# Optimization experiments

Hardware: AMD Instinct MI355X
Metric: run time of the kernel (lower is better)

Reference implementation:

```python
import jax, jax.numpy as jnp
import numpy as np
from functools import partial

SIZES = (32.0, 64.0, 128.0, 256.0, 512.0)
RATIOS = (0.5, 1.0, 2.0)
POS_T, NEG_T = 0.7, 0.3


def _make_anchors(img_size, grid_sizes):
    # Mirrors AnchorGenerator: per feature, per size, per ratio, grid-flattened.
    parts = []
    for g in grid_sizes:
        stride = img_size / g
        steps = jnp.arange(g, dtype=jnp.float32) * stride
        x, y = jnp.meshgrid(steps, steps, indexing='ij')  # torch default 'ij'
        for s in SIZES:
            for r in RATIOS:
                rs = float(np.sqrt(r))
                wa = jnp.full((g, g), s * rs, jnp.float32)
                ha = jnp.full((g, g), s / rs, jnp.float32)
                parts.append(jnp.stack((x, y, wa, ha), axis=-1).reshape(-1, 4))
    return jnp.concatenate(parts, axis=0)  # [R,4] (cx,cy,w,h)


def _conv(x, w, b, pad):
    y = jax.lax.conv_general_dilated(x, w, (1, 1), [(pad, pad), (pad, pad)],
                                     dimension_numbers=('NCHW', 'OIHW', 'NCHW'))
    return y + b[None, :, None, None]


def _head(feat, conv_w, conv_b, cls_w, cls_b, box_w, box_b):
    t = jax.nn.relu(_conv(feat, conv_w, conv_b, 1))
    logits = _conv(t, cls_w, cls_b, 0)   # [b,A,g,g]
    bbox = _conv(t, box_w, box_b, 0)     # [b,4A,g,g]
    b, A, g, _ = logits.shape
    logits = logits.reshape(b, -1)       # [b, A*g*g] (anchor-major, matches anchor order)
    bbox = bbox.reshape(b, A, 4, g, g).transpose(0, 1, 3, 4, 2).reshape(b, -1, 4)
    return logits, bbox


def _iou(a, b):
    # a [R,4] xyxy, b [N,4] xyxy -> [R,N]
    lt = jnp.maximum(a[:, None, :2], b[None, :, :2])
    rb = jnp.minimum(a[:, None, 2:], b[None, :, 2:])
    wh = jnp.clip(rb - lt, 0.0)
    inter = wh[..., 0] * wh[..., 1]
    area_a = (a[:, 2] - a[:, 0]) * (a[:, 3] - a[:, 1])
    area_b = (b[:, 2] - b[:, 0]) * (b[:, 3] - b[:, 1])
    return inter / (area_a[:, None] + area_b[None, :] - inter)


def _label_one(anchors_xyxy, gt_xywh):
    # label_anchors for a single image
    gt = jnp.concatenate([gt_xywh[:, :2], gt_xywh[:, :2] + gt_xywh[:, 2:]], axis=-1)
    iou = _iou(anchors_xyxy, gt)               # [R,N]
    score = iou.max(axis=1)
    matched = gt[jnp.argmax(iou, axis=1)]      # [R,4]
    pos = score > POS_T
    pos = pos.at[jnp.argmax(iou, axis=0)].set(True)  # best anchor per gt
    labels = jnp.where(score < NEG_T, 0.0, jnp.where(pos, 1.0, -1.0))
    return labels, matched


def _forward(images, feats, gt_boxes, conv_w, conv_b, cls_w, cls_b, box_w, box_b):
    grid_sizes = [f.shape[-1] for f in feats]
    anchors = _make_anchors(float(images.shape[-1]), grid_sizes)  # [R,4] cwh
    half = anchors[:, 2:] * 0.5
    anchors_xyxy = jnp.concatenate([anchors[:, :2] - half, anchors[:, :2] + half], -1)
    outs = [_head(f, conv_w, conv_b, cls_w, cls_b, box_w, box_b) for f in feats]
    obj = jnp.concatenate([o for o, _ in outs], axis=1)      # [b,R]
    deltas = jnp.concatenate([d for _, d in outs], axis=1)   # [b,R,4]
    labels, matched = jax.vmap(partial(_label_one, anchors_xyxy))(gt_boxes)
    preds = jnp.concatenate([obj[..., None], deltas], axis=-1)  # [b,R,5]
    return preds, labels, matched


def setup_inputs() -> dict:
    key = jax.random.key(0)
    ks = jax.random.split(key, 12)
    b, C, A = 2, 256, 15
    grids = (128, 64, 32, 16, 8)
    inp = {'images': jax.random.uniform(ks[0], (b, 3, 512, 512), jnp.float32)}
    for i, g in enumerate(grids):
        inp[f'feat{i}'] = jax.random.normal(ks[1 + i], (b, C, g, g), jnp.float32)
    xy = jax.random.uniform(ks[6], (b, 32, 2), jnp.float32) * 384.0
    wh = 16.0 + jax.random.uniform(ks[7], (b, 32, 2), jnp.float32) * 112.0
    inp['gt_boxes'] = jnp.concatenate([xy, wh], axis=-1)  # (x,y,w,h)
    inp['conv_w'] = 0.01 * jax.random.normal(ks[8], (C, C, 3, 3), jnp.float32)
    inp['conv_b'] = jnp.zeros((C,), jnp.float32)
    inp['cls_w'] = 0.01 * jax.random.normal(ks[9], (A, C, 1, 1), jnp.float32)
    inp['cls_b'] = jnp.zeros((A,), jnp.float32)
    inp['box_w'] = 0.01 * jax.random.normal(ks[10], (4 * A, C, 1, 1), jnp.float32)
    inp['box_b'] = jnp.zeros((4 * A,), jnp.float32)
    return inp


def reference(images, feat0, feat1, feat2, feat3, feat4, gt_boxes,
              conv_w, conv_b, cls_w, cls_b, box_w, box_b):
    return _forward(images, [feat0, feat1, feat2, feat3, feat4], gt_boxes,
                    conv_w, conv_b, cls_w, cls_b, box_w, box_b)
```

## Files before the change

kernel.cpp:

```cpp
#include <hip/hip_runtime.h>

typedef unsigned short u16;
typedef unsigned char  u8;
typedef unsigned int   u32;
typedef __bf16 bf16x8 __attribute__((ext_vector_type(8)));
typedef float  f32x4  __attribute__((ext_vector_type(4)));
typedef u16    u16x8  __attribute__((ext_vector_type(8)));
typedef u16    u16x4  __attribute__((ext_vector_type(4)));

#define R_TOTAL 327360
#define LAB_OFF 3273600
#define MAT_OFF 3928320
#define NLBLK   1279

static __device__ const int    D_LOG2G[5] = {7, 6, 5, 4, 3};
static __device__ const size_t D_FTOFF[5] = {0, 8389120, 10486784, 11011584, 11143168};
static __device__ const int    D_TPOFF[5] = {0, 32768, 40960, 43008, 43520};
static __device__ const int    D_AOFF[5]  = {0, 245760, 307200, 322560, 326400};

static __device__ const float D_WH[15][2] = {
  {22.627416997969522f, 45.254833995939045f}, {32.f, 32.f},   {45.254833995939045f, 22.627416997969522f},
  {45.254833995939045f, 90.50966799187809f},  {64.f, 64.f},   {90.50966799187809f, 45.254833995939045f},
  {90.50966799187809f, 181.01933598375618f},  {128.f, 128.f}, {181.01933598375618f, 90.50966799187809f},
  {181.01933598375618f, 362.03867196751236f}, {256.f, 256.f}, {362.03867196751236f, 181.01933598375618f},
  {362.03867196751236f, 724.0773439350247f},  {512.f, 512.f}, {724.0773439350247f, 362.03867196751236f},
};

__device__ __forceinline__ u16 f2bf(float x) {
  u32 u = __float_as_uint(x);
  u32 r = u + 0x7FFFu + ((u >> 16) & 1u);
  return (u16)(r >> 16);
}
__device__ __forceinline__ float bf2f(u16 v) { return __uint_as_float(((u32)v) << 16); }

__device__ __forceinline__ void glds16(const void* g, void* l) {
  __builtin_amdgcn_global_load_lds(
      (const __attribute__((address_space(1))) u32*)g,
      (__attribute__((address_space(3))) u32*)l, 16, 0, 0);
}

__device__ inline void anchor_box(int r, float& x1, float& y1, float& x2, float& y2) {
  #pragma clang fp contract(off)
  int off, lg;
  if (r < 245760)      { off = 0;      lg = 7; }
  else if (r < 307200) { off = 245760; lg = 6; }
  else if (r < 322560) { off = 307200; lg = 5; }
  else if (r < 326400) { off = 322560; lg = 4; }
  else                 { off = 326400; lg = 3; }
  int rem  = r - off;
  int a    = rem >> (2 * lg);
  int rem2 = rem & ((1 << (2 * lg)) - 1);
  int i = rem2 >> lg;
  int j = rem2 & ((1 << lg) - 1);
  float stride = (float)(512 >> lg);
  float cx = (float)i * stride;
  float cy = (float)j * stride;
  float hw = D_WH[a][0] * 0.5f;
  float hh = D_WH[a][1] * 0.5f;
  x1 = cx - hw; y1 = cy - hh; x2 = cx + hw; y2 = cy + hh;
}

__device__ inline float iou_f(float ax1, float ay1, float ax2, float ay2,
                              float bx1, float by1, float bx2, float by2) {
  #pragma clang fp contract(off)
  float ltx = fmaxf(ax1, bx1), lty = fmaxf(ay1, by1);
  float rbx = fminf(ax2, bx2), rby = fminf(ay2, by2);
  float iw = fmaxf(rbx - ltx, 0.f);
  float ih = fmaxf(rby - lty, 0.f);
  float inter = iw * ih;
  float aa = (ax2 - ax1) * (ay2 - ay1);
  float ab = (bx2 - bx1) * (by2 - by1);
  return inter / (aa + ab - inter);
}

__global__ __launch_bounds__(256) void pack_all_kernel(
    const float* __restrict__ cw, u16* __restrict__ wp,
    const float* __restrict__ cls_w, const float* __restrict__ cls_b,
    const float* __restrict__ box_w, const float* __restrict__ box_b,
    u16* __restrict__ Wb, float* __restrict__ hbias) {
  if (blockIdx.x < 2304) {
    int idx = blockIdx.x * 256 + threadIdx.x;
    int ks  = idx >> 13;
    int rem = idx & 8191;
    int co  = rem >> 5;
    int k   = rem & 31;
    int tap = ks >> 3;
    int cb  = ks & 7;
    float v = cw[co * 2304 + (cb * 32 + k) * 9 + tap];
    int qd = k >> 3, wi = k & 7;
    int dq = qd ^ ((co >> 1) & 3);
    wp[(size_t)ks * 8192 + co * 32 + dq * 8 + wi] = f2bf(v);
  } else {
    int idx = (blockIdx.x - 2304) * 256 + threadIdx.x;
    int row = idx >> 8, k = idx & 255;
    float v = (row < 15) ? cls_w[row * 256 + k] : (row < 75) ? box_w[(row - 15) * 256 + k] : 0.f;
    Wb[row * 256 + k] = f2bf(v);
    if (idx < 80) hbias[idx] = (idx < 15) ? cls_b[idx] : (idx < 75) ? box_b[idx - 15] : 0.f;
  }
}

__global__ __launch_bounds__(256) void feat_pack_kernel(
    const float* __restrict__ f0, const float* __restrict__ f1,
    const float* __restrict__ f2, const float* __restrict__ f3,
    const float* __restrict__ f4, u16* __restrict__ Ft) {
  __shared__ float tile[64][65];
  int bid = blockIdx.x;
  int l, base, nb1;
  if (bid < 514)      { l = 0; base = 0;   nb1 = 257; }
  else if (bid < 644) { l = 1; base = 514; nb1 = 65; }
  else if (bid < 678) { l = 2; base = 644; nb1 = 17; }
  else if (bid < 688) { l = 3; base = 678; nb1 = 5; }
  else                { l = 4; base = 688; nb1 = 2; }
  const int lg = D_LOG2G[l];
  const int HW = 1 << (2 * lg);
  int blk = bid - base;
  int b   = blk / nb1;
  int p0  = (blk - b * nb1) * 64;
  u16* dst = Ft + D_FTOFF[l];
  const int tid = threadIdx.x;
  if (p0 >= HW) {
    if (tid < 32) {
      u16x8 z = (u16x8)0;
      *(u16x8*)(dst + ((size_t)b * (HW + 1) + HW) * 256 + tid * 8) = z;
    }
    return;
  }
  const float* fsel = (l == 0) ? f0 : (l == 1) ? f1 : (l == 2) ? f2 : (l == 3) ? f3 : f4;
  const float* fb = fsel + (size_t)b * 256 * HW;
  for (int cg = 0; cg < 4; ++cg) {
    __syncthreads();
    #pragma unroll
    for (int i = 0; i < 16; ++i) {
      int idx = i * 256 + tid;
      int cl = idx >> 6, pp = idx & 63;
      tile[cl][pp] = fb[(size_t)(cg * 64 + cl) * HW + p0 + pp];
    }
    __syncthreads();
    #pragma unroll
    for (int i = 0; i < 2; ++i) {
      int slot = i * 256 + tid;
      int pos = slot >> 3, ch = slot & 7;
      u16x8 v;
      #pragma unroll
      for (int j = 0; j < 8; ++j) v[j] = f2bf(tile[ch * 8 + j][pos]);
      *(u16x8*)(dst + ((size_t)b * (HW + 1) + p0 + pos) * 256 + cg * 64 + ch * 8) = v;
    }
  }
}

__global__ __launch_bounds__(128) void conv_mfma_kernel(
    const u16* __restrict__ Ft, const u16* __restrict__ wp,
    const float* __restrict__ cb, u16* __restrict__ tP) {
  __shared__ __align__(16) u8 Asb[16384];
  __shared__ __align__(16) u8 Bsb[8192];
  const int bid = blockIdx.x;
  int l, base;
  if (bid < 1024)      { l = 0; base = 0; }
  else if (bid < 1280) { l = 1; base = 1024; }
  else if (bid < 1344) { l = 2; base = 1280; }
  else if (bid < 1360) { l = 3; base = 1344; }
  else                 { l = 4; base = 1360; }
  const int lg = D_LOG2G[l];
  const int g = 1 << lg, HW = 1 << (2 * lg);
  const int lognt = 2 * lg - 5;
  const int blk = bid - base;
  const int ct = blk >> lognt;
  const int tile = blk & ((1 << lognt) - 1);
  const int n0 = tile << 6;
  const int co0 = ct << 7;
  const int tid = threadIdx.x;
  const int wv = tid >> 6, lane = tid & 63;
  const u16* FtL = Ft + D_FTOFF[l];
  const u8* wpb = (const u8*)wp;
  const int b_img = n0 >> (2 * lg);
  const int dq = tid & 3;
  const int nl0 = tid >> 2, nl1 = nl0 + 32;
  const int swz0 = (dq ^ ((nl0 >> 1) & 3)) << 3;
  const int swz1 = (dq ^ ((nl1 >> 1) & 3)) << 3;
  const int pg0 = (n0 + nl0) & (HW - 1);
  const int h0 = pg0 >> lg, w0 = pg0 & (g - 1);
  const int pg1 = (n0 + nl1) & (HW - 1);
  const int h1 = pg1 >> lg, w1 = pg1 & (g - 1);
  const u16* bimg = FtL + (size_t)b_img * (HW + 1) * 256;
  const int lm = lane & 15, lq = lane >> 4;
  int aoffs[4], boffs[4];
  #pragma unroll
  for (int mi = 0; mi < 4; ++mi) {
    int row = wv * 64 + mi * 16 + lm;
    aoffs[mi] = row * 64 + ((lq ^ ((row >> 1) & 3)) << 4);
  }
  #pragma unroll
  for (int ni = 0; ni < 4; ++ni) {
    int col = ni * 16 + lm;
    boffs[ni] = col * 64 + ((lq ^ ((col >> 1) & 3)) << 4);
  }
  f32x4 acc[4][4];
  #pragma unroll
  for (int mi = 0; mi < 4; ++mi)
    #pragma unroll
    for (int ni = 0; ni < 4; ++ni) acc[mi][ni] = (f32x4)0.f;

  auto tap_src = [&](int tap, const u16*& s0, const u16*& s1) {
    const int dh = tap / 3 - 1, dw = tap % 3 - 1;
    int sh0 = h0 + dh, sw0 = w0 + dw;
    int r0 = ((unsigned)sh0 < (unsigned)g && (unsigned)sw0 < (unsigned)g) ? (sh0 * g + sw0) : HW;
    int sh1 = h1 + dh, sw1 = w1 + dw;
    int r1 = ((unsigned)sh1 < (unsigned)g && (unsigned)sw1 < (unsigned)g) ? (sh1 * g + sw1) : HW;
    s0 = bimg + (size_t)r0 * 256 + swz0;
    s1 = bimg + (size_t)r1 * 256 + swz1;
  };
  auto STAGE = [&](int p, int tap_, int cb8_, const u16* s0, const u16* s1) {
    glds16(s0 + cb8_ * 32, Bsb + p * 4096 + wv * 1024);
    glds16(s1 + cb8_ * 32, Bsb + p * 4096 + (2 + wv) * 1024);
    const u8* aK = wpb + (size_t)(tap_ * 8 + cb8_) * 16384 + co0 * 64;
    #pragma unroll
    for (int c = 0; c < 4; ++c) {
      int ch = c * 2 + wv;
      glds16(aK + ch * 1024 + lane * 16, Asb + p * 8192 + ch * 1024);
    }
  };

  const u16 *cs0, *cs1;
  tap_src(0, cs0, cs1);
  int p = 0;
  STAGE(0, 0, 0, cs0, cs1);
  __syncthreads();

  for (int tap = 0; tap < 9; ++tap) {
    const u16 *ns0 = cs0, *ns1 = cs1;
    if (tap < 8) tap_src(tap + 1, ns0, ns1);
    #pragma unroll
    for (int cb8 = 0; cb8 < 8; ++cb8) {
      if (!(tap == 8 && cb8 == 7)) {
        if (cb8 < 7) STAGE(p ^ 1, tap, cb8 + 1, cs0, cs1);
        else         STAGE(p ^ 1, tap + 1, 0, ns0, ns1);
      }
      bf16x8 af[4], bfr[4];
      #pragma unroll
      for (int mi = 0; mi < 4; ++mi) af[mi] = *(const bf16x8*)(Asb + p * 8192 + aoffs[mi]);
      #pragma unroll
      for (int ni = 0; ni < 4; ++ni) bfr[ni] = *(const bf16x8*)(Bsb + p * 4096 + boffs[ni]);
      #pragma unroll
      for (int mi = 0; mi < 4; ++mi)
        #pragma unroll
        for (int ni = 0; ni < 4; ++ni)
          acc[mi][ni] = __builtin_amdgcn_mfma_f32_16x16x32_bf16(af[mi], bfr[ni], acc[mi][ni], 0, 0, 0);
      __syncthreads();
      p ^= 1;
    }
    cs0 = ns0; cs1 = ns1;
  }
  u16* tPL = tP + ((size_t)D_TPOFF[l] + (size_t)b_img * HW) * 256;
  #pragma unroll
  for (int mi = 0; mi < 4; ++mi) {
    const int cob = co0 + wv * 64 + mi * 16 + lq * 4;
    const float4 bs = *(const float4*)&cb[cob];
    #pragma unroll
    for (int ni = 0; ni < 4; ++ni) {
      int pp = (n0 + ni * 16 + lm) & (HW - 1);
      u16x4 v;
      v[0] = f2bf(fmaxf(acc[mi][ni][0] + bs.x, 0.f));
      v[1] = f2bf(fmaxf(acc[mi][ni][1] + bs.y, 0.f));
      v[2] = f2bf(fmaxf(acc[mi][ni][2] + bs.z, 0.f));
      v[3] = f2bf(fmaxf(acc[mi][ni][3] + bs.w, 0.f));
      *(u16x4*)&tPL[(size_t)pp * 256 + cob] = v;
    }
  }
}

__global__ __launch_bounds__(128) void head_mfma_kernel(
    const u16* __restrict__ tP, const u16* __restrict__ Wb,
    const float* __restrict__ hbias, float* __restrict__ out) {
  __shared__ __align__(16) u8 Bsb[32768];
  const int bid = blockIdx.x;
  int l, base;
  if (bid < 512)      { l = 0; base = 0; }
  else if (bid < 640) { l = 1; base = 512; }
  else if (bid < 672) { l = 2; base = 640; }
  else if (bid < 680) { l = 3; base = 672; }
  else                { l = 4; base = 680; }
  const int lg = D_LOG2G[l];
  const int HW = 1 << (2 * lg);
  const int blk = bid - base;
  const int n0 = blk << 6;
  const int tid = threadIdx.x;
  const int wv = tid >> 6, lane = tid & 63;
  const int lm = lane & 15, lq = lane >> 4;
  const u16* src = tP + ((size_t)D_TPOFF[l] + n0) * 256;
  #pragma unroll
  for (int i = 0; i < 16; ++i) {
    int c = wv + i * 2;
    int slot = c * 64 + lane;
    int pos = slot >> 5, sp = slot & 31;
    glds16(src + (size_t)pos * 256 + ((sp ^ (pos & 7)) << 3), Bsb + c * 1024);
  }
  __syncthreads();
  f32x4 acc[5][2];
  #pragma unroll
  for (int mi = 0; mi < 5; ++mi) { acc[mi][0] = (f32x4)0.f; acc[mi][1] = (f32x4)0.f; }
  for (int kb = 0; kb < 8; ++kb) {
    bf16x8 af[5], bfr[2];
    #pragma unroll
    for (int mi = 0; mi < 5; ++mi)
      af[mi] = *(const bf16x8*)&Wb[(mi * 16 + lm) * 256 + kb * 32 + lq * 8];
    #pragma unroll
    for (int ni = 0; ni < 2; ++ni) {
      int p_ = wv * 32 + ni * 16 + lm;
      bfr[ni] = *(const bf16x8*)(Bsb + p_ * 512 + (((kb * 4 + lq) ^ (p_ & 7)) << 4));
    }
    #pragma unroll
    for (int mi = 0; mi < 5; ++mi)
      #pragma unroll
      for (int ni = 0; ni < 2; ++ni)
        acc[mi][ni] = __builtin_amdgcn_mfma_f32_16x16x32_bf16(af[mi], bfr[ni], acc[mi][ni], 0, 0, 0);
  }
  const int b   = n0 >> (2 * lg);
  const int pgb = n0 & (HW - 1);
  const size_t obase = (size_t)b * R_TOTAL;
  const int aoff = D_AOFF[l];
  #pragma unroll
  for (int mi = 0; mi < 5; ++mi) {
    #pragma unroll
    for (int r = 0; r < 4; ++r) {
      int oc = mi * 16 + lq * 4 + r;
      if (oc < 75) {
        float bs = hbias[oc];
        size_t rr; int comp;
        if (oc < 15) { rr = (size_t)aoff + (size_t)oc * HW; comp = 0; }
        else { int o2 = oc - 15; rr = (size_t)aoff + (size_t)(o2 >> 2) * HW; comp = 1 + (o2 & 3); }
        #pragma unroll
        for (int ni = 0; ni < 2; ++ni) {
          int pg = pgb + wv * 32 + ni * 16 + lm;
          out[(obase + rr + pg) * 5 + comp] = acc[mi][ni][r] + bs;
        }
      }
    }
  }
}

__global__ __launch_bounds__(256) void label_fused_kernel(const float* __restrict__ gt,
                                                          float* __restrict__ out,
                                                          float2* __restrict__ partial) {
  #pragma clang fp contract(off)
  __shared__ float gx[32][4];
  __shared__ float sh[256][33];
  __shared__ float2 red[32][8];
  const int b = blockIdx.y;
  const int tid = threadIdx.x;
  if (tid < 32) {
    const float* gp = gt + ((size_t)b * 32 + tid) * 4;
    float x = gp[0], y = gp[1], w = gp[2], h = gp[3];
    gx[tid][0] = x; gx[tid][1] = y; gx[tid][2] = x + w; gx[tid][3] = y + h;
  }
  __syncthreads();
  const int r = blockIdx.x * 256 + tid;
  const bool valid = (r < R_TOTAL);
  const int rv = valid ? r : 0;
  float ax1, ay1, ax2, ay2;
  anchor_box(rv, ax1, ay1, ax2, ay2);
  float best = -1e30f; int bi = 0;
  for (int n = 0; n < 32; ++n) {
    float v = iou_f(ax1, ay1, ax2, ay2, gx[n][0], gx[n][1], gx[n][2], gx[n][3]);
    sh[tid][n] = valid ? v : -1e30f;
    if (v > best) { best = v; bi = n; }
  }
  if (valid) {
    float lab = (best < 0.3f) ? 0.f : ((best > 0.7f) ? 1.f : -1.f);
    out[LAB_OFF + (size_t)b * R_TOTAL + r] = lab;
    float4 m; m.x = gx[bi][0]; m.y = gx[bi][1]; m.z = gx[bi][2]; m.w = gx[bi][3];
    *(float4*)&out[MAT_OFF + ((size_t)b * R_TOTAL + r) * 4] = m;
  }
  __syncthreads();
  const int n = tid & 31, gr = tid >> 5;
  float bv = -1e30f; int li = 0;
  #pragma unroll 4
  for (int a = 0; a < 32; ++a) {
    int la = gr * 32 + a;
    float v = sh[la][n];
    if (v > bv) { bv = v; li = la; }
  }
  red[n][gr] = make_float2(bv, __int_as_float(li));
  __syncthreads();
  if (tid < 32) {
    float fv = -1e30f; int fi = 0;
    #pragma unroll
    for (int g2 = 0; g2 < 8; ++g2) {
      float2 pv = red[tid][g2];
      int ii = __float_as_int(pv.y);
      if (pv.x > fv) { fv = pv.x; fi = ii; }
    }
    partial[(size_t)(b * 32 + tid) * NLBLK + blockIdx.x] =
        make_float2(fv, __int_as_float(blockIdx.x * 256 + fi));
  }
}

__global__ __launch_bounds__(256) void argmax_final2_kernel(
    const float* __restrict__ gt, const float2* __restrict__ partial,
    float* __restrict__ out) {
  #pragma clang fp contract(off)
  __shared__ float sv[256];
  __shared__ int   si[256];
  const int b = blockIdx.x >> 5, n = blockIdx.x & 31;
  const float2* pp = partial + (size_t)(b * 32 + n) * NLBLK;
  const int tid = threadIdx.x;
  float bv = -1e30f; int bi = 0x7fffffff;
  for (int i = tid; i < NLBLK; i += 256) {
    float2 pv = pp[i]; int ii = __float_as_int(pv.y);
    if (pv.x > bv || (pv.x == bv && ii < bi)) { bv = pv.x; bi = ii; }
  }
  sv[tid] = bv; si[tid] = bi;
  __syncthreads();
  for (int s = 128; s > 0; s >>= 1) {
    if (tid < s) {
      float v2 = sv[tid + s]; int i2 = si[tid + s];
      if (v2 > sv[tid] || (v2 == sv[tid] && i2 < si[tid])) { sv[tid] = v2; si[tid] = i2; }
    }
    __syncthreads();
  }
  if (tid == 0) {
    int banch = si[0];
    float ax1, ay1, ax2, ay2;
    anchor_box(banch, ax1, ay1, ax2, ay2);
    float score = -1e30f;
    for (int n2 = 0; n2 < 32; ++n2) {
      const float* gp = gt + ((size_t)b * 32 + n2) * 4;
      float v = iou_f(ax1, ay1, ax2, ay2, gp[0], gp[1], gp[0] + gp[2], gp[1] + gp[3]);
      score = fmaxf(score, v);
    }
    out[LAB_OFF + (size_t)b * R_TOTAL + banch] = (score < 0.3f) ? 0.f : 1.f;
  }
}

extern "C" void kernel_launch(void* const* d_in, const int* in_sizes, int n_in,
                              void* d_out, int out_size, void* d_ws, size_t ws_size,
                              hipStream_t stream) {
  const float* f0     = (const float*)d_in[1];
  const float* f1     = (const float*)d_in[2];
  const float* f2     = (const float*)d_in[3];
  const float* f3     = (const float*)d_in[4];
  const float* f4     = (const float*)d_in[5];
  const float* gt     = (const float*)d_in[6];
  const float* conv_w = (const float*)d_in[7];
  const float* conv_b = (const float*)d_in[8];
  const float* cls_w  = (const float*)d_in[9];
  const float* cls_b  = (const float*)d_in[10];
  const float* box_w  = (const float*)d_in[11];
  const float* box_b  = (const float*)d_in[12];
  float* out = (float*)d_out;
  u8* wsb = (u8*)d_ws;

  u16*    wp      = (u16*)wsb;
  u16*    Ft      = (u16*)(wsb + 1179648);
  u16*    tP      = (u16*)(wsb + 23532544);
  u16*    Wb      = (u16*)(wsb + 45880320);
  float*  hbias   = (float*)(wsb + 45921280);
  float2* partial = (float2*)(wsb + 45921600);

  pack_all_kernel<<<2384, 256, 0, stream>>>(conv_w, wp, cls_w, cls_b, box_w, box_b, Wb, hbias);
  feat_pack_kernel<<<692, 256, 0, stream>>>(f0, f1, f2, f3, f4, Ft);
  conv_mfma_kernel<<<1364, 128, 0, stream>>>(Ft, wp, conv_b, tP);
  head_mfma_kernel<<<682, 128, 0, stream>>>(tP, Wb, hbias, out);
  label_fused_kernel<<<dim3(NLBLK, 2), 256, 0, stream>>>(gt, out, partial);
  argmax_final2_kernel<<<64, 256, 0, stream>>>(gt, partial, out);
}
```

Baseline: 231.6 us.

## Enlarge conv tile to 128x128 with 4 waves and merge prep kernels

The conv MFMA kernel moves from 128 threads computing a 128x64 output tile to 256 threads (2x2 waves) computing a 128x128 tile. The B pixel tile can now span both images, so each pixel row tracks its own image index. This halves the block count and reuses each staged weight tile across twice as many pixels, cutting global weight traffic per output. The weight-pack and feature-pack kernels are also merged into one launch to save a launch gap. The cost is fewer blocks (682) to fill the GPU's compute units and larger LDS use per block.

```diff
diff --git a/kernel.cpp b/kernel.cpp
--- a/kernel.cpp
+++ b/kernel.cpp
@@ -73,13 +73,18 @@
   return inter / (aa + ab - inter);
 }
 
-__global__ __launch_bounds__(256) void pack_all_kernel(
+__global__ __launch_bounds__(256) void prep_kernel(
     const float* __restrict__ cw, u16* __restrict__ wp,
     const float* __restrict__ cls_w, const float* __restrict__ cls_b,
     const float* __restrict__ box_w, const float* __restrict__ box_b,
-    u16* __restrict__ Wb, float* __restrict__ hbias) {
+    u16* __restrict__ Wb, float* __restrict__ hbias,
+    const float* __restrict__ f0, const float* __restrict__ f1,
+    const float* __restrict__ f2, const float* __restrict__ f3,
+    const float* __restrict__ f4, u16* __restrict__ Ft) {
+  __shared__ float tile[64][65];
+  const int tid = threadIdx.x;
   if (blockIdx.x < 2304) {
-    int idx = blockIdx.x * 256 + threadIdx.x;
+    int idx = blockIdx.x * 256 + tid;
     int ks  = idx >> 13;
     int rem = idx & 8191;
     int co  = rem >> 5;
@@ -90,21 +95,17 @@
     int qd = k >> 3, wi = k & 7;
     int dq = qd ^ ((co >> 1) & 3);
     wp[(size_t)ks * 8192 + co * 32 + dq * 8 + wi] = f2bf(v);
-  } else {
-    int idx = (blockIdx.x - 2304) * 256 + threadIdx.x;
+    return;
+  }
+  if (blockIdx.x < 2384) {
+    int idx = (blockIdx.x - 2304) * 256 + tid;
     int row = idx >> 8, k = idx & 255;
     float v = (row < 15) ? cls_w[row * 256 + k] : (row < 75) ? box_w[(row - 15) * 256 + k] : 0.f;
     Wb[row * 256 + k] = f2bf(v);
     if (idx < 80) hbias[idx] = (idx < 15) ? cls_b[idx] : (idx < 75) ? box_b[idx - 15] : 0.f;
-  }
-}
-
-__global__ __launch_bounds__(256) void feat_pack_kernel(
-    const float* __restrict__ f0, const float* __restrict__ f1,
-    const float* __restrict__ f2, const float* __restrict__ f3,
-    const float* __restrict__ f4, u16* __restrict__ Ft) {
-  __shared__ float tile[64][65];
-  int bid = blockIdx.x;
+    return;
+  }
+  int bid = blockIdx.x - 2384;
   int l, base, nb1;
   if (bid < 514)      { l = 0; base = 0;   nb1 = 257; }
   else if (bid < 644) { l = 1; base = 514; nb1 = 65; }
@@ -117,7 +118,6 @@
   int b   = blk / nb1;
   int p0  = (blk - b * nb1) * 64;
   u16* dst = Ft + D_FTOFF[l];
-  const int tid = threadIdx.x;
   if (p0 >= HW) {
     if (tid < 32) {
       u16x8 z = (u16x8)0;
@@ -148,50 +148,53 @@
   }
 }
 
-__global__ __launch_bounds__(128) void conv_mfma_kernel(
+__global__ __launch_bounds__(256) void conv_mfma_kernel(
     const u16* __restrict__ Ft, const u16* __restrict__ wp,
     const float* __restrict__ cb, u16* __restrict__ tP) {
   __shared__ __align__(16) u8 Asb[16384];
-  __shared__ __align__(16) u8 Bsb[8192];
+  __shared__ __align__(16) u8 Bsb[16384];
   const int bid = blockIdx.x;
   int l, base;
-  if (bid < 1024)      { l = 0; base = 0; }
-  else if (bid < 1280) { l = 1; base = 1024; }
-  else if (bid < 1344) { l = 2; base = 1280; }
-  else if (bid < 1360) { l = 3; base = 1344; }
-  else                 { l = 4; base = 1360; }
+  if (bid < 512)      { l = 0; base = 0; }
+  else if (bid < 640) { l = 1; base = 512; }
+  else if (bid < 672) { l = 2; base = 640; }
+  else if (bid < 680) { l = 3; base = 672; }
+  else                { l = 4; base = 680; }
   const int lg = D_LOG2G[l];
   const int g = 1 << lg, HW = 1 << (2 * lg);
-  const int lognt = 2 * lg - 5;
+  const int lognt = 2 * lg - 6;
   const int blk = bid - base;
   const int ct = blk >> lognt;
   const int tile = blk & ((1 << lognt) - 1);
-  const int n0 = tile << 6;
+  const int n0 = tile << 7;
   const int co0 = ct << 7;
   const int tid = threadIdx.x;
   const int wv = tid >> 6, lane = tid & 63;
+  const int wr = wv >> 1, wc = wv & 1;
   const u16* FtL = Ft + D_FTOFF[l];
   const u8* wpb = (const u8*)wp;
-  const int b_img = n0 >> (2 * lg);
-  const int dq = tid & 3;
-  const int nl0 = tid >> 2, nl1 = nl0 + 32;
-  const int swz0 = (dq ^ ((nl0 >> 1) & 3)) << 3;
-  const int swz1 = (dq ^ ((nl1 >> 1) & 3)) << 3;
-  const int pg0 = (n0 + nl0) & (HW - 1);
-  const int h0 = pg0 >> lg, w0 = pg0 & (g - 1);
-  const int pg1 = (n0 + nl1) & (HW - 1);
-  const int h1 = pg1 >> lg, w1 = pg1 & (g - 1);
-  const u16* bimg = FtL + (size_t)b_img * (HW + 1) * 256;
+  const int dq = lane & 3;
+  const int rB0 = wv * 32 + (lane >> 2);
+  const int rB1 = rB0 + 16;
+  int bI0, h0, w0, bI1, h1, w1, q0, q1;
+  {
+    int pf0 = n0 + rB0; bI0 = pf0 >> (2 * lg); int p0_ = pf0 & (HW - 1);
+    h0 = p0_ >> lg; w0 = p0_ & (g - 1); q0 = dq ^ ((rB0 >> 1) & 3);
+    int pf1 = n0 + rB1; bI1 = pf1 >> (2 * lg); int p1_ = pf1 & (HW - 1);
+    h1 = p1_ >> lg; w1 = p1_ & (g - 1); q1 = dq ^ ((rB1 >> 1) & 3);
+  }
+  const size_t img0 = (size_t)bI0 * (HW + 1), img1 = (size_t)bI1 * (HW + 1);
+  const u8* pA = wpb + (size_t)co0 * 64 + (size_t)(wv * 32 + (lane >> 2)) * 64 + dq * 16;
   const int lm = lane & 15, lq = lane >> 4;
   int aoffs[4], boffs[4];
   #pragma unroll
   for (int mi = 0; mi < 4; ++mi) {
-    int row = wv * 64 + mi * 16 + lm;
+    int row = wr * 64 + mi * 16 + lm;
     aoffs[mi] = row * 64 + ((lq ^ ((row >> 1) & 3)) << 4);
   }
   #pragma unroll
   for (int ni = 0; ni < 4; ++ni) {
-    int col = ni * 16 + lm;
+    int col = wc * 64 + ni * 16 + lm;
     boffs[ni] = col * 64 + ((lq ^ ((col >> 1) & 3)) << 4);
   }
   f32x4 acc[4][4];
@@ -206,18 +209,15 @@
     int r0 = ((unsigned)sh0 < (unsigned)g && (unsigned)sw0 < (unsigned)g) ? (sh0 * g + sw0) : HW;
     int sh1 = h1 + dh, sw1 = w1 + dw;
     int r1 = ((unsigned)sh1 < (unsigned)g && (unsigned)sw1 < (unsigned)g) ? (sh1 * g + sw1) : HW;
-    s0 = bimg + (size_t)r0 * 256 + swz0;
-    s1 = bimg + (size_t)r1 * 256 + swz1;
+    s0 = FtL + (img0 + r0) * 256 + q0 * 8;
+    s1 = FtL + (img1 + r1) * 256 + q1 * 8;
   };
-  auto STAGE = [&](int p, int tap_, int cb8_, const u16* s0, const u16* s1) {
-    glds16(s0 + cb8_ * 32, Bsb + p * 4096 + wv * 1024);
-    glds16(s1 + cb8_ * 32, Bsb + p * 4096 + (2 + wv) * 1024);
-    const u8* aK = wpb + (size_t)(tap_ * 8 + cb8_) * 16384 + co0 * 64;
-    #pragma unroll
-    for (int c = 0; c < 4; ++c) {
-      int ch = c * 2 + wv;
-      glds16(aK + ch * 1024 + lane * 16, Asb + p * 8192 + ch * 1024);
-    }
+  auto STAGE = [&](int p, int ks, int cb8, const u16* s0, const u16* s1) {
+    glds16(s0 + cb8 * 32, Bsb + p * 8192 + wv * 2048);
+    glds16(s1 + cb8 * 32, Bsb + p * 8192 + wv * 2048 + 1024);
+    const u8* aK = pA + (size_t)ks * 16384;
+    glds16(aK,        Asb + p * 8192 + wv * 2048);
+    glds16(aK + 1024, Asb + p * 8192 + wv * 2048 + 1024);
   };
 
   const u16 *cs0, *cs1;
@@ -232,14 +232,14 @@
     #pragma unroll
     for (int cb8 = 0; cb8 < 8; ++cb8) {
       if (!(tap == 8 && cb8 == 7)) {
-        if (cb8 < 7) STAGE(p ^ 1, tap, cb8 + 1, cs0, cs1);
-        else         STAGE(p ^ 1, tap + 1, 0, ns0, ns1);
+        if (cb8 < 7) STAGE(p ^ 1, tap * 8 + cb8 + 1, cb8 + 1, cs0, cs1);
+        else         STAGE(p ^ 1, (tap + 1) * 8, 0, ns0, ns1);
       }
       bf16x8 af[4], bfr[4];
       #pragma unroll
       for (int mi = 0; mi < 4; ++mi) af[mi] = *(const bf16x8*)(Asb + p * 8192 + aoffs[mi]);
       #pragma unroll
-      for (int ni = 0; ni < 4; ++ni) bfr[ni] = *(const bf16x8*)(Bsb + p * 4096 + boffs[ni]);
+      for (int ni = 0; ni < 4; ++ni) bfr[ni] = *(const bf16x8*)(Bsb + p * 8192 + boffs[ni]);
       #pragma unroll
       for (int mi = 0; mi < 4; ++mi)
         #pragma unroll
@@ -250,20 +250,22 @@
     }
     cs0 = ns0; cs1 = ns1;
   }
-  u16* tPL = tP + ((size_t)D_TPOFF[l] + (size_t)b_img * HW) * 256;
+  const u16* tPL = tP + (size_t)D_TPOFF[l] * 256;
   #pragma unroll
   for (int mi = 0; mi < 4; ++mi) {
-    const int cob = co0 + wv * 64 + mi * 16 + lq * 4;
+    const int cob = co0 + wr * 64 + mi * 16 + lq * 4;
     const float4 bs = *(const float4*)&cb[cob];
     #pragma unroll
     for (int ni = 0; ni < 4; ++ni) {
-      int pp = (n0 + ni * 16 + lm) & (HW - 1);
+      int pf = n0 + wc * 64 + ni * 16 + lm;
+      int bI = pf >> (2 * lg);
+      int pp = pf & (HW - 1);
       u16x4 v;
       v[0] = f2bf(fmaxf(acc[mi][ni][0] + bs.x, 0.f));
       v[1] = f2bf(fmaxf(acc[mi][ni][1] + bs.y, 0.f));
       v[2] = f2bf(fmaxf(acc[mi][ni][2] + bs.z, 0.f));
       v[3] = f2bf(fmaxf(acc[mi][ni][3] + bs.w, 0.f));
-      *(u16x4*)&tPL[(size_t)pp * 256 + cob] = v;
+      *(u16x4*)&((u16*)tPL)[((size_t)bI * HW + pp) * 256 + cob] = v;
     }
   }
 }
@@ -456,9 +458,9 @@
   float*  hbias   = (float*)(wsb + 45921280);
   float2* partial = (float2*)(wsb + 45921600);
 
-  pack_all_kernel<<<2384, 256, 0, stream>>>(conv_w, wp, cls_w, cls_b, box_w, box_b, Wb, hbias);
-  feat_pack_kernel<<<692, 256, 0, stream>>>(f0, f1, f2, f3, f4, Ft);
-  conv_mfma_kernel<<<1364, 128, 0, stream>>>(Ft, wp, conv_b, tP);
+  prep_kernel<<<3076, 256, 0, stream>>>(conv_w, wp, cls_w, cls_b, box_w, box_b,
+                                        Wb, hbias, f0, f1, f2, f3, f4, Ft);
+  conv_mfma_kernel<<<682, 256, 0, stream>>>(Ft, wp, conv_b, tP);
   head_mfma_kernel<<<682, 128, 0, stream>>>(tP, Wb, hbias, out);
   label_fused_kernel<<<dim3(NLBLK, 2), 256, 0, stream>>>(gt, out, partial);
   argmax_final2_kernel<<<64, 256, 0, stream>>>(gt, partial, out);
```

New measurement: 270.3 us. +16.7%, slower.

## Merge prep, feature pack and labeling into one launch; widen conv blocks

Applied to the files above, without the earlier changes.

The weight packing, feature transpose/pack and anchor labeling kernels become one launch partitioned by block index. The separate argmax-final kernel is replaced by 64-bit atomicMax keys plus a last-block-done counter, which needs a small memset per call. The conv kernel moves from 128 to 256 threads with a 2x2 wave layout, so each wave computes a 64x32 sub-tile and stages fewer global-to-LDS loads. The aim is to cut launch count and tail idle time and to improve conv occupancy, at the cost of atomic contention and a changed argmax tie-break (smallest index wins via complemented key).

```diff
diff --git a/kernel.cpp b/kernel.cpp
--- a/kernel.cpp
+++ b/kernel.cpp
@@ -3,6 +3,7 @@
 typedef unsigned short u16;
 typedef unsigned char  u8;
 typedef unsigned int   u32;
+typedef unsigned long long u64;
 typedef __bf16 bf16x8 __attribute__((ext_vector_type(8)));
 typedef float  f32x4  __attribute__((ext_vector_type(4)));
 typedef u16    u16x8  __attribute__((ext_vector_type(8)));
@@ -31,7 +32,6 @@
   u32 r = u + 0x7FFFu + ((u >> 16) & 1u);
   return (u16)(r >> 16);
 }
-__device__ __forceinline__ float bf2f(u16 v) { return __uint_as_float(((u32)v) << 16); }
 
 __device__ __forceinline__ void glds16(const void* g, void* l) {
   __builtin_amdgcn_global_load_lds(
@@ -73,13 +73,28 @@
   return inter / (aa + ab - inter);
 }
 
-__global__ __launch_bounds__(256) void pack_all_kernel(
+__global__ __launch_bounds__(256) void prep_label_kernel(
     const float* __restrict__ cw, u16* __restrict__ wp,
     const float* __restrict__ cls_w, const float* __restrict__ cls_b,
     const float* __restrict__ box_w, const float* __restrict__ box_b,
-    u16* __restrict__ Wb, float* __restrict__ hbias) {
+    u16* __restrict__ Wb, float* __restrict__ hbias,
+    const float* __restrict__ f0, const float* __restrict__ f1,
+    const float* __restrict__ f2, const float* __restrict__ f3,
+    const float* __restrict__ f4, u16* __restrict__ Ft,
+    const float* __restrict__ gt, float* __restrict__ out,
+    u64* __restrict__ win, u32* __restrict__ done) {
+  __shared__ union {
+    float tile[64][65];
+    struct {
+      float gx[32][4];
+      float sh[256][33];
+      float2 red[32][8];
+    } L;
+  } sm;
+  __shared__ int lastFlag;
+  const int tid = threadIdx.x;
   if (blockIdx.x < 2304) {
-    int idx = blockIdx.x * 256 + threadIdx.x;
+    int idx = blockIdx.x * 256 + tid;
     int ks  = idx >> 13;
     int rem = idx & 8191;
     int co  = rem >> 5;
@@ -90,65 +105,138 @@
     int qd = k >> 3, wi = k & 7;
     int dq = qd ^ ((co >> 1) & 3);
     wp[(size_t)ks * 8192 + co * 32 + dq * 8 + wi] = f2bf(v);
-  } else {
-    int idx = (blockIdx.x - 2304) * 256 + threadIdx.x;
+    return;
+  }
+  if (blockIdx.x < 2384) {
+    int idx = (blockIdx.x - 2304) * 256 + tid;
     int row = idx >> 8, k = idx & 255;
     float v = (row < 15) ? cls_w[row * 256 + k] : (row < 75) ? box_w[(row - 15) * 256 + k] : 0.f;
     Wb[row * 256 + k] = f2bf(v);
     if (idx < 80) hbias[idx] = (idx < 15) ? cls_b[idx] : (idx < 75) ? box_b[idx - 15] : 0.f;
-  }
-}
-
-__global__ __launch_bounds__(256) void feat_pack_kernel(
-    const float* __restrict__ f0, const float* __restrict__ f1,
-    const float* __restrict__ f2, const float* __restrict__ f3,
-    const float* __restrict__ f4, u16* __restrict__ Ft) {
-  __shared__ float tile[64][65];
-  int bid = blockIdx.x;
-  int l, base, nb1;
-  if (bid < 514)      { l = 0; base = 0;   nb1 = 257; }
-  else if (bid < 644) { l = 1; base = 514; nb1 = 65; }
-  else if (bid < 678) { l = 2; base = 644; nb1 = 17; }
-  else if (bid < 688) { l = 3; base = 678; nb1 = 5; }
-  else                { l = 4; base = 688; nb1 = 2; }
-  const int lg = D_LOG2G[l];
-  const int HW = 1 << (2 * lg);
-  int blk = bid - base;
-  int b   = blk / nb1;
-  int p0  = (blk - b * nb1) * 64;
-  u16* dst = Ft + D_FTOFF[l];
-  const int tid = threadIdx.x;
-  if (p0 >= HW) {
+    return;
+  }
+  if (blockIdx.x < 3076) {
+    int bid = blockIdx.x - 2384;
+    int l, base, nb1;
+    if (bid < 514)      { l = 0; base = 0;   nb1 = 257; }
+    else if (bid < 644) { l = 1; base = 514; nb1 = 65; }
+    else if (bid < 678) { l = 2; base = 644; nb1 = 17; }
+    else if (bid < 688) { l = 3; base = 678; nb1 = 5; }
+    else                { l = 4; base = 688; nb1 = 2; }
+    const int lg = D_LOG2G[l];
+    const int HW = 1 << (2 * lg);
+    int blk = bid - base;
+    int b   = blk / nb1;
+    int p0  = (blk - b * nb1) * 64;
+    u16* dst = Ft + D_FTOFF[l];
+    if (p0 >= HW) {
+      if (tid < 32) {
+        u16x8 z = (u16x8)0;
+        *(u16x8*)(dst + ((size_t)b * (HW + 1) + HW) * 256 + tid * 8) = z;
+      }
+      return;
+    }
+    const float* fsel = (l == 0) ? f0 : (l == 1) ? f1 : (l == 2) ? f2 : (l == 3) ? f3 : f4;
+    const float* fb = fsel + (size_t)b * 256 * HW;
+    for (int cg = 0; cg < 4; ++cg) {
+      __syncthreads();
+      #pragma unroll
+      for (int i = 0; i < 16; ++i) {
+        int idx = i * 256 + tid;
+        int cl = idx >> 6, pp = idx & 63;
+        sm.tile[cl][pp] = fb[(size_t)(cg * 64 + cl) * HW + p0 + pp];
+      }
+      __syncthreads();
+      #pragma unroll
+      for (int i = 0; i < 2; ++i) {
+        int slot = i * 256 + tid;
+        int pos = slot >> 3, ch = slot & 7;
+        u16x8 v;
+        #pragma unroll
+        for (int j = 0; j < 8; ++j) v[j] = f2bf(sm.tile[ch * 8 + j][pos]);
+        *(u16x8*)(dst + ((size_t)b * (HW + 1) + p0 + pos) * 256 + cg * 64 + ch * 8) = v;
+      }
+    }
+    return;
+  }
+  {
+    #pragma clang fp contract(off)
+    const int lb = blockIdx.x - 3076;
+    const int b = (lb >= NLBLK) ? 1 : 0;
+    const int lblk = lb - b * NLBLK;
     if (tid < 32) {
-      u16x8 z = (u16x8)0;
-      *(u16x8*)(dst + ((size_t)b * (HW + 1) + HW) * 256 + tid * 8) = z;
-    }
-    return;
-  }
-  const float* fsel = (l == 0) ? f0 : (l == 1) ? f1 : (l == 2) ? f2 : (l == 3) ? f3 : f4;
-  const float* fb = fsel + (size_t)b * 256 * HW;
-  for (int cg = 0; cg < 4; ++cg) {
+      const float* gp = gt + ((size_t)b * 32 + tid) * 4;
+      float x = gp[0], y = gp[1], w = gp[2], h = gp[3];
+      sm.L.gx[tid][0] = x; sm.L.gx[tid][1] = y;
+      sm.L.gx[tid][2] = x + w; sm.L.gx[tid][3] = y + h;
+    }
     __syncthreads();
-    #pragma unroll
-    for (int i = 0; i < 16; ++i) {
-      int idx = i * 256 + tid;
-      int cl = idx >> 6, pp = idx & 63;
-      tile[cl][pp] = fb[(size_t)(cg * 64 + cl) * HW + p0 + pp];
+    const int r = lblk * 256 + tid;
+    const bool valid = (r < R_TOTAL);
+    const int rv = valid ? r : 0;
+    float ax1, ay1, ax2, ay2;
+    anchor_box(rv, ax1, ay1, ax2, ay2);
+    float best = -1e30f; int bi = 0;
+    for (int n = 0; n < 32; ++n) {
+      float v = iou_f(ax1, ay1, ax2, ay2, sm.L.gx[n][0], sm.L.gx[n][1], sm.L.gx[n][2], sm.L.gx[n][3]);
+      sm.L.sh[tid][n] = valid ? v : -1e30f;
+      if (v > best) { best = v; bi = n; }
+    }
+    if (valid) {
+      float lab = (best < 0.3f) ? 0.f : ((best > 0.7f) ? 1.f : -1.f);
+      out[LAB_OFF + (size_t)b * R_TOTAL + r] = lab;
+      float4 m; m.x = sm.L.gx[bi][0]; m.y = sm.L.gx[bi][1];
+      m.z = sm.L.gx[bi][2]; m.w = sm.L.gx[bi][3];
+      *(float4*)&out[MAT_OFF + ((size_t)b * R_TOTAL + r) * 4] = m;
     }
     __syncthreads();
-    #pragma unroll
-    for (int i = 0; i < 2; ++i) {
-      int slot = i * 256 + tid;
-      int pos = slot >> 3, ch = slot & 7;
-      u16x8 v;
-      #pragma unroll
-      for (int j = 0; j < 8; ++j) v[j] = f2bf(tile[ch * 8 + j][pos]);
-      *(u16x8*)(dst + ((size_t)b * (HW + 1) + p0 + pos) * 256 + cg * 64 + ch * 8) = v;
-    }
-  }
-}
-
-__global__ __launch_bounds__(128) void conv_mfma_kernel(
+    const int n = tid & 31, gr = tid >> 5;
+    float bv = -1e30f; int li = 0;
+    #pragma unroll 4
+    for (int a = 0; a < 32; ++a) {
+      int la = gr * 32 + a;
+      float v = sm.L.sh[la][n];
+      if (v > bv) { bv = v; li = la; }
+    }
+    sm.L.red[n][gr] = make_float2(bv, __int_as_float(li));
+    __syncthreads();
+    if (tid < 32) {
+      float fv = -1e30f; int fi = 0;
+      #pragma unroll
+      for (int g2 = 0; g2 < 8; ++g2) {
+        float2 pv = sm.L.red[tid][g2];
+        int ii = __float_as_int(pv.y);
+        if (pv.x > fv) { fv = pv.x; fi = ii; }
+      }
+      u64 key = ((u64)__float_as_uint(fv) << 32) |
+                (u64)(0xFFFFFFFFu - (u32)(lblk * 256 + fi));
+      atomicMax(&win[b * 32 + tid], key);
+    }
+    __threadfence();
+    __syncthreads();
+    if (tid == 0) {
+      u32 old = atomicAdd(&done[b], 1u);
+      lastFlag = (old == NLBLK - 1) ? 1 : 0;
+    }
+    __syncthreads();
+    if (lastFlag && tid < 32) {
+      u64 k = atomicMax(&win[b * 32 + tid], 0ull);
+      u32 hi = (u32)(k >> 32);
+      int ra = hi ? (int)(0xFFFFFFFFu - (u32)k) : 0;
+      float x1, y1, x2, y2;
+      anchor_box(ra, x1, y1, x2, y2);
+      float score = -1e30f;
+      for (int n2 = 0; n2 < 32; ++n2) {
+        float v = iou_f(x1, y1, x2, y2, sm.L.gx[n2][0], sm.L.gx[n2][1],
+                        sm.L.gx[n2][2], sm.L.gx[n2][3]);
+        score = fmaxf(score, v);
+      }
+      out[LAB_OFF + (size_t)b * R_TOTAL + ra] = (score < 0.3f) ? 0.f : 1.f;
+    }
+  }
+}
+
+__global__ __launch_bounds__(256) void conv_mfma_kernel(
     const u16* __restrict__ Ft, const u16* __restrict__ wp,
     const float* __restrict__ cb, u16* __restrict__ tP) {
   __shared__ __align__(16) u8 Asb[16384];
@@ -170,94 +258,83 @@
   const int co0 = ct << 7;
   const int tid = threadIdx.x;
   const int wv = tid >> 6, lane = tid & 63;
+  const int wr = wv >> 1, wc = wv & 1;
   const u16* FtL = Ft + D_FTOFF[l];
   const u8* wpb = (const u8*)wp;
   const int b_img = n0 >> (2 * lg);
   const int dq = tid & 3;
-  const int nl0 = tid >> 2, nl1 = nl0 + 32;
-  const int swz0 = (dq ^ ((nl0 >> 1) & 3)) << 3;
-  const int swz1 = (dq ^ ((nl1 >> 1) & 3)) << 3;
-  const int pg0 = (n0 + nl0) & (HW - 1);
-  const int h0 = pg0 >> lg, w0 = pg0 & (g - 1);
-  const int pg1 = (n0 + nl1) & (HW - 1);
-  const int h1 = pg1 >> lg, w1 = pg1 & (g - 1);
+  const int rB = tid >> 2;
+  const int pgb = (n0 + rB) & (HW - 1);
+  const int h0 = pgb >> lg, w0 = pgb & (g - 1);
+  const int q0 = dq ^ ((rB >> 1) & 3);
   const u16* bimg = FtL + (size_t)b_img * (HW + 1) * 256;
   const int lm = lane & 15, lq = lane >> 4;
-  int aoffs[4], boffs[4];
+  int aoffs[4], boffs[2];
   #pragma unroll
   for (int mi = 0; mi < 4; ++mi) {
-    int row = wv * 64 + mi * 16 + lm;
+    int row = wr * 64 + mi * 16 + lm;
     aoffs[mi] = row * 64 + ((lq ^ ((row >> 1) & 3)) << 4);
   }
   #pragma unroll
-  for (int ni = 0; ni < 4; ++ni) {
-    int col = ni * 16 + lm;
+  for (int ni = 0; ni < 2; ++ni) {
+    int col = wc * 32 + ni * 16 + lm;
     boffs[ni] = col * 64 + ((lq ^ ((col >> 1) & 3)) << 4);
   }
-  f32x4 acc[4][4];
+  f32x4 acc[4][2];
   #pragma unroll
   for (int mi = 0; mi < 4; ++mi)
     #pragma unroll
-    for (int ni = 0; ni < 4; ++ni) acc[mi][ni] = (f32x4)0.f;
-
-  auto tap_src = [&](int tap, const u16*& s0, const u16*& s1) {
+    for (int ni = 0; ni < 2; ++ni) acc[mi][ni] = (f32x4)0.f;
+
+  auto tap_src = [&](int tap) -> const u16* {
     const int dh = tap / 3 - 1, dw = tap % 3 - 1;
-    int sh0 = h0 + dh, sw0 = w0 + dw;
-    int r0 = ((unsigned)sh0 < (unsigned)g && (unsigned)sw0 < (unsigned)g) ? (sh0 * g + sw0) : HW;
-    int sh1 = h1 + dh, sw1 = w1 + dw;
-    int r1 = ((unsigned)sh1 < (unsigned)g && (unsigned)sw1 < (unsigned)g) ? (sh1 * g + sw1) : HW;
-    s0 = bimg + (size_t)r0 * 256 + swz0;
-    s1 = bimg + (size_t)r1 * 256 + swz1;
+    int sh = h0 + dh, sw = w0 + dw;
+    int rr = ((unsigned)sh < (unsigned)g && (unsigned)sw < (unsigned)g) ? (sh * g + sw) : HW;
+    return bimg + (size_t)rr * 256 + q0 * 8;
   };
-  auto STAGE = [&](int p, int tap_, int cb8_, const u16* s0, const u16* s1) {
-    glds16(s0 + cb8_ * 32, Bsb + p * 4096 + wv * 1024);
-    glds16(s1 + cb8_ * 32, Bsb + p * 4096 + (2 + wv) * 1024);
-    const u8* aK = wpb + (size_t)(tap_ * 8 + cb8_) * 16384 + co0 * 64;
-    #pragma unroll
-    for (int c = 0; c < 4; ++c) {
-      int ch = c * 2 + wv;
-      glds16(aK + ch * 1024 + lane * 16, Asb + p * 8192 + ch * 1024);
-    }
+  auto STAGE = [&](int p, int ks, int cb8, const u16* s0) {
+    glds16(s0 + cb8 * 32, Bsb + p * 4096 + wv * 1024);
+    const u8* aK = wpb + (size_t)ks * 16384 + co0 * 64;
+    glds16(aK + wv * 1024 + lane * 16,       Asb + p * 8192 + wv * 1024);
+    glds16(aK + (4 + wv) * 1024 + lane * 16, Asb + p * 8192 + (4 + wv) * 1024);
   };
 
-  const u16 *cs0, *cs1;
-  tap_src(0, cs0, cs1);
+  const u16* cs0 = tap_src(0);
   int p = 0;
-  STAGE(0, 0, 0, cs0, cs1);
+  STAGE(0, 0, 0, cs0);
   __syncthreads();
 
   for (int tap = 0; tap < 9; ++tap) {
-    const u16 *ns0 = cs0, *ns1 = cs1;
-    if (tap < 8) tap_src(tap + 1, ns0, ns1);
+    const u16* ns0 = (tap < 8) ? tap_src(tap + 1) : cs0;
     #pragma unroll
     for (int cb8 = 0; cb8 < 8; ++cb8) {
       if (!(tap == 8 && cb8 == 7)) {
-        if (cb8 < 7) STAGE(p ^ 1, tap, cb8 + 1, cs0, cs1);
-        else         STAGE(p ^ 1, tap + 1, 0, ns0, ns1);
-      }
-      bf16x8 af[4], bfr[4];
+        if (cb8 < 7) STAGE(p ^ 1, tap * 8 + cb8 + 1, cb8 + 1, cs0);
+        else         STAGE(p ^ 1, (tap + 1) * 8, 0, ns0);
+      }
+      bf16x8 af[4], bfr[2];
       #pragma unroll
       for (int mi = 0; mi < 4; ++mi) af[mi] = *(const bf16x8*)(Asb + p * 8192 + aoffs[mi]);
       #pragma unroll
-      for (int ni = 0; ni < 4; ++ni) bfr[ni] = *(const bf16x8*)(Bsb + p * 4096 + boffs[ni]);
+      for (int ni = 0; ni < 2; ++ni) bfr[ni] = *(const bf16x8*)(Bsb + p * 4096 + boffs[ni]);
       #pragma unroll
       for (int mi = 0; mi < 4; ++mi)
         #pragma unroll
-        for (int ni = 0; ni < 4; ++ni)
+        for (int ni = 0; ni < 2; ++ni)
           acc[mi][ni] = __builtin_amdgcn_mfma_f32_16x16x32_bf16(af[mi], bfr[ni], acc[mi][ni], 0, 0, 0);
       __syncthreads();
       p ^= 1;
     }
-    cs0 = ns0; cs1 = ns1;
+    cs0 = ns0;
   }
   u16* tPL = tP + ((size_t)D_TPOFF[l] + (size_t)b_img * HW) * 256;
   #pragma unroll
   for (int mi = 0; mi < 4; ++mi) {
-    const int cob = co0 + wv * 64 + mi * 16 + lq * 4;
+    const int cob = co0 + wr * 64 + mi * 16 + lq * 4;
     const float4 bs = *(const float4*)&cb[cob];
     #pragma unroll
-    for (int ni = 0; ni < 4; ++ni) {
-      int pp = (n0 + ni * 16 + lm) & (HW - 1);
+    for (int ni = 0; ni < 2; ++ni) {
+      int pp = (n0 + wc * 32 + ni * 16 + lm) & (HW - 1);
       u16x4 v;
       v[0] = f2bf(fmaxf(acc[mi][ni][0] + bs.x, 0.f));
       v[1] = f2bf(fmaxf(acc[mi][ni][1] + bs.y, 0.f));
@@ -338,99 +415,6 @@
   }
 }
 
-__global__ __launch_bounds__(256) void label_fused_kernel(const float* __restrict__ gt,
-                                                          float* __restrict__ out,
-                                                          float2* __restrict__ partial) {
-  #pragma clang fp contract(off)
-  __shared__ float gx[32][4];
-  __shared__ float sh[256][33];
-  __shared__ float2 red[32][8];
-  const int b = blockIdx.y;
-  const int tid = threadIdx.x;
-  if (tid < 32) {
-    const float* gp = gt + ((size_t)b * 32 + tid) * 4;
-    float x = gp[0], y = gp[1], w = gp[2], h = gp[3];
-    gx[tid][0] = x; gx[tid][1] = y; gx[tid][2] = x + w; gx[tid][3] = y + h;
-  }
-  __syncthreads();
-  const int r = blockIdx.x * 256 + tid;
-  const bool valid = (r < R_TOTAL);
-  const int rv = valid ? r : 0;
-  float ax1, ay1, ax2, ay2;
-  anchor_box(rv, ax1, ay1, ax2, ay2);
-  float best = -1e30f; int bi = 0;
-  for (int n = 0; n < 32; ++n) {
-    float v = iou_f(ax1, ay1, ax2, ay2, gx[n][0], gx[n][1], gx[n][2], gx[n][3]);
-    sh[tid][n] = valid ? v : -1e30f;
-    if (v > best) { best = v; bi = n; }
-  }
-  if (valid) {
-    float lab = (best < 0.3f) ? 0.f : ((best > 0.7f) ? 1.f : -1.f);
-    out[LAB_OFF + (size_t)b * R_TOTAL + r] = lab;
-    float4 m; m.x = gx[bi][0]; m.y = gx[bi][1]; m.z = gx[bi][2]; m.w = gx[bi][3];
-    *(float4*)&out[MAT_OFF + ((size_t)b * R_TOTAL + r) * 4] = m;
-  }
-  __syncthreads();
-  const int n = tid & 31, gr = tid >> 5;
-  float bv = -1e30f; int li = 0;
-  #pragma unroll 4
-  for (int a = 0; a < 32; ++a) {
-    int la = gr * 32 + a;
-    float v = sh[la][n];
-    if (v > bv) { bv = v; li = la; }
-  }
-  red[n][gr] = make_float2(bv, __int_as_float(li));
-  __syncthreads();
-  if (tid < 32) {
-    float fv = -1e30f; int fi = 0;
-    #pragma unroll
-    for (int g2 = 0; g2 < 8; ++g2) {
-      float2 pv = red[tid][g2];
-      int ii = __float_as_int(pv.y);
-      if (pv.x > fv) { fv = pv.x; fi = ii; }
-    }
-    partial[(size_t)(b * 32 + tid) * NLBLK + blockIdx.x] =
-        make_float2(fv, __int_as_float(blockIdx.x * 256 + fi));
-  }
-}
-
-__global__ __launch_bounds__(256) void argmax_final2_kernel(
-    const float* __restrict__ gt, const float2* __restrict__ partial,
-    float* __restrict__ out) {
-  #pragma clang fp contract(off)
-  __shared__ float sv[256];
-  __shared__ int   si[256];
-  const int b = blockIdx.x >> 5, n = blockIdx.x & 31;
-  const float2* pp = partial + (size_t)(b * 32 + n) * NLBLK;
-  const int tid = threadIdx.x;
-  float bv = -1e30f; int bi = 0x7fffffff;
-  for (int i = tid; i < NLBLK; i += 256) {
-    float2 pv = pp[i]; int ii = __float_as_int(pv.y);
-    if (pv.x > bv || (pv.x == bv && ii < bi)) { bv = pv.x; bi = ii; }
-  }
-  sv[tid] = bv; si[tid] = bi;
-  __syncthreads();
-  for (int s = 128; s > 0; s >>= 1) {
-    if (tid < s) {
-      float v2 = sv[tid + s]; int i2 = si[tid + s];
-      if (v2 > sv[tid] || (v2 == sv[tid] && i2 < si[tid])) { sv[tid] = v2; si[tid] = i2; }
-    }
-    __syncthreads();
-  }
-  if (tid == 0) {
-    int banch = si[0];
-    float ax1, ay1, ax2, ay2;
-    anchor_box(banch, ax1, ay1, ax2, ay2);
-    float score = -1e30f;
-    for (int n2 = 0; n2 < 32; ++n2) {
-      const float* gp = gt + ((size_t)b * 32 + n2) * 4;
-      float v = iou_f(ax1, ay1, ax2, ay2, gp[0], gp[1], gp[0] + gp[2], gp[1] + gp[3]);
-      score = fmaxf(score, v);
-    }
-    out[LAB_OFF + (size_t)b * R_TOTAL + banch] = (score < 0.3f) ? 0.f : 1.f;
-  }
-}
-
 extern "C" void kernel_launch(void* const* d_in, const int* in_sizes, int n_in,
                               void* d_out, int out_size, void* d_ws, size_t ws_size,
                               hipStream_t stream) {
@@ -449,17 +433,18 @@
   float* out = (float*)d_out;
   u8* wsb = (u8*)d_ws;
 
-  u16*    wp      = (u16*)wsb;
-  u16*    Ft      = (u16*)(wsb + 1179648);
-  u16*    tP      = (u16*)(wsb + 23532544);
-  u16*    Wb      = (u16*)(wsb + 45880320);
-  float*  hbias   = (float*)(wsb + 45921280);
-  float2* partial = (float2*)(wsb + 45921600);
-
-  pack_all_kernel<<<2384, 256, 0, stream>>>(conv_w, wp, cls_w, cls_b, box_w, box_b, Wb, hbias);
-  feat_pack_kernel<<<692, 256, 0, stream>>>(f0, f1, f2, f3, f4, Ft);
-  conv_mfma_kernel<<<1364, 128, 0, stream>>>(Ft, wp, conv_b, tP);
+  u16*   wp    = (u16*)wsb;
+  u16*   Ft    = (u16*)(wsb + 1179648);
+  u16*   tP    = (u16*)(wsb + 23532544);
+  u16*   Wb    = (u16*)(wsb + 45880320);
+  float* hbias = (float*)(wsb + 45921280);
+  u64*   win   = (u64*)(wsb + 45921600);
+  u32*   done  = (u32*)(wsb + 45922112);
+
+  (void)hipMemsetAsync(wsb + 45921600, 0, 520, stream);
+  prep_label_kernel<<<5634, 256, 0, stream>>>(conv_w, wp, cls_w, cls_b, box_w, box_b,
+                                              Wb, hbias, f0, f1, f2, f3, f4, Ft,
+                                              gt, out, win, done);
+  conv_mfma_kernel<<<1364, 256, 0, stream>>>(Ft, wp, conv_b, tP);
   head_mfma_kernel<<<682, 128, 0, stream>>>(tP, Wb, hbias, out);
-  label_fused_kernel<<<dim3(NLBLK, 2), 256, 0, stream>>>(gt, out, partial);
-  argmax_final2_kernel<<<64, 256, 0, stream>>>(gt, partial, out);
-}
+}
```

Result: slower. 447.7 us (+93.3%).
